# Performance work log

Measured on AMD Instinct MI355X. Metric: run time of the kernel, lower is better.

Reference implementation:

```python
import jax, jax.numpy as jnp
import numpy as np
import math

D_MODEL = 512
NUM_HEADS = 8
D_HEAD = D_MODEL // NUM_HEADS
B, S = 8, 1024


def _rel_shift(pos_score):
    # pos_score: [B, H, S, S] -> Transformer-XL relative shift
    b, h, s1, s2 = pos_score.shape
    padded = jnp.concatenate([jnp.zeros((b, h, s1, 1), pos_score.dtype), pos_score], axis=-1)
    padded = padded.reshape(b, h, s2 + 1, s1)
    return padded[:, :, 1:].reshape(b, h, s1, s2)


def setup_inputs() -> dict:
    key = jax.random.key(0)
    ks = jax.random.split(key, 16)
    scale = 1.0 / math.sqrt(D_MODEL)
    inp = {
        'query': jax.random.normal(ks[0], (B, S, D_MODEL), jnp.float32),
        'key': jax.random.normal(ks[1], (B, S, D_MODEL), jnp.float32),
        'value': jax.random.normal(ks[2], (B, S, D_MODEL), jnp.float32),
        'position_emb': jax.random.normal(ks[3], (B, S, D_MODEL), jnp.float32),
        'Wq': jax.random.normal(ks[4], (D_MODEL, D_MODEL), jnp.float32) * scale,
        'bq': jnp.zeros((D_MODEL,), jnp.float32),
        'Wk': jax.random.normal(ks[5], (D_MODEL, D_MODEL), jnp.float32) * scale,
        'bk': jnp.zeros((D_MODEL,), jnp.float32),
        'Wv': jax.random.normal(ks[6], (D_MODEL, D_MODEL), jnp.float32) * scale,
        'bv': jnp.zeros((D_MODEL,), jnp.float32),
        'Wp': jax.random.normal(ks[7], (D_MODEL, D_MODEL), jnp.float32) * scale,
        'u_bias': jax.random.normal(ks[8], (NUM_HEADS, D_HEAD), jnp.float32) * 0.1,
        'v_bias': jax.random.normal(ks[9], (NUM_HEADS, D_HEAD), jnp.float32) * 0.1,
        'Wo': jax.random.normal(ks[10], (D_MODEL, D_MODEL), jnp.float32) * scale,
        'bo': jnp.zeros((D_MODEL,), jnp.float32),
    }
    return inp


def reference(query, key, value, position_emb, Wq, bq, Wk, bk, Wv, bv, Wp, u_bias, v_bias, Wo, bo):
    b, s, _ = query.shape
    q = (query @ Wq + bq).reshape(b, s, NUM_HEADS, D_HEAD)       # [B,S,H,Dh]
    k = (key @ Wk + bk).reshape(b, s, NUM_HEADS, D_HEAD)
    v = (value @ Wv + bv).reshape(b, s, NUM_HEADS, D_HEAD)
    p = (position_emb @ Wp).reshape(b, s, NUM_HEADS, D_HEAD)
    # content score: (q + u) k^T ; pos score: (q + v) p^T with relative shift
    content_score = jnp.einsum('bqhd,bkhd->bhqk', q + u_bias, k)
    pos_score = _rel_shift(jnp.einsum('bqhd,bkhd->bhqk', q + v_bias, p))
    score = (content_score + pos_score) / math.sqrt(D_MODEL)
    atten = jax.nn.softmax(score, axis=-1)                        # dropout off (eval)
    context = jnp.einsum('bhqk,bkhd->bqhd', atten, v).reshape(b, s, D_MODEL)
    return context @ Wo + bo
```

## Files before the change

### kernel.cpp

```cpp
#include <hip/hip_runtime.h>
#include <cstdint>

typedef unsigned short ushort_t;
typedef __attribute__((ext_vector_type(8))) short bf16x8;
typedef __attribute__((ext_vector_type(4))) float f32x4;

#define S_LEN 1024
#define DHEAD 64

__device__ inline ushort_t f2bf(float f) {
    union { float f; uint32_t u; } c; c.f = f;
    uint32_t u = c.u;
    uint32_t r = u + 0x7FFFu + ((u >> 16) & 1u);
    return (ushort_t)(r >> 16);
}
__device__ inline float bf2f(ushort_t h) {
    union { uint32_t u; float f; } c; c.u = ((uint32_t)h) << 16;
    return c.f;
}
__device__ inline bf16x8 load8(const ushort_t* p) {
    union { uint4 u; bf16x8 v; } c;
    c.u = *reinterpret_cast<const uint4*>(p);
    return c.v;
}

__global__ __launch_bounds__(256) void prep_w(
    const float* __restrict__ wq, const float* __restrict__ wk,
    const float* __restrict__ wv, const float* __restrict__ wp,
    const float* __restrict__ wo, ushort_t* __restrict__ ws) {
    __shared__ float tile[64][65];
    int wi = blockIdx.z;
    const float* src = wi == 0 ? wq : wi == 1 ? wk : wi == 2 ? wv : wi == 3 ? wp : wo;
    int cx = blockIdx.x * 64, ry = blockIdx.y * 64;
    int t = threadIdx.x;
    int tr = t >> 4, tc = (t & 15) * 4;
#pragma unroll
    for (int i = 0; i < 4; i++) {
        int r = tr + i * 16;
        float4 f = *reinterpret_cast<const float4*>(src + (size_t)(ry + r) * 512 + cx + tc);
        tile[r][tc] = f.x; tile[r][tc + 1] = f.y; tile[r][tc + 2] = f.z; tile[r][tc + 3] = f.w;
    }
    __syncthreads();
    ushort_t* dst = ws + (size_t)wi * 262144;
#pragma unroll
    for (int i = 0; i < 4; i++) {
        int r = tr + i * 16;
        ushort4 o;
        o.x = f2bf(tile[tc][r]); o.y = f2bf(tile[tc + 1][r]);
        o.z = f2bf(tile[tc + 2][r]); o.w = f2bf(tile[tc + 3][r]);
        *reinterpret_cast<ushort4*>(dst + (size_t)(cx + r) * 512 + ry + tc) = o;
    }
}

__global__ __launch_bounds__(256) void prep_act(
    const float* __restrict__ q, const float* __restrict__ k,
    const float* __restrict__ v, const float* __restrict__ p,
    ushort_t* __restrict__ actb) {
    int t = blockIdx.x * 256 + threadIdx.x;
    int sec = blockIdx.y;
    const float* src = sec == 0 ? q : sec == 1 ? k : sec == 2 ? v : p;
    ushort_t* dst = actb + (size_t)sec * 4194304;
    float4 f = reinterpret_cast<const float4*>(src)[t];
    ushort4 o;
    o.x = f2bf(f.x); o.y = f2bf(f.y); o.z = f2bf(f.z); o.w = f2bf(f.w);
    *reinterpret_cast<ushort4*>(dst + (size_t)t * 4) = o;
}

template<int CVT>
__global__ __launch_bounds__(256) void proj_gemm(
    const float* __restrict__ qa, const float* __restrict__ ka,
    const float* __restrict__ va, const float* __restrict__ pa,
    const ushort_t* __restrict__ actb,
    const ushort_t* __restrict__ wT,
    const float* __restrict__ bq, const float* __restrict__ bk,
    const float* __restrict__ bv,
    const float* __restrict__ ub, const float* __restrict__ vb,
    ushort_t* __restrict__ Qu, ushort_t* __restrict__ Qv,
    ushort_t* __restrict__ Kp, ushort_t* __restrict__ Pp,
    ushort_t* __restrict__ Vt) {
    __shared__ ushort_t smem[2][128][72];
    int z = blockIdx.z;
    const float* Af = z == 0 ? qa : z == 1 ? ka : z == 2 ? pa : va;
    const ushort_t* Ab = actb + (size_t)(z == 0 ? 0 : z == 1 ? 1 : z == 2 ? 3 : 2) * 4194304;
    const ushort_t* Bt = wT + (z == 0 ? 0 : z == 1 ? 262144 : z == 2 ? 786432 : 524288);
    const float* bias = z == 0 ? bq : z == 1 ? bk : z == 3 ? bv : nullptr;

    int tid = threadIdx.x;
    int wid = tid >> 6, lane = tid & 63, quad = lane >> 4, l16 = lane & 15;
    int wr = wid >> 1, wc = wid & 1;
    int row0 = blockIdx.y * 128, col0 = blockIdx.x * 128;

    f32x4 acc[4][4];
#pragma unroll
    for (int i = 0; i < 4; i++)
#pragma unroll
        for (int j = 0; j < 4; j++) acc[i][j] = (f32x4){0.f, 0.f, 0.f, 0.f};

    for (int k0 = 0; k0 < 512; k0 += 64) {
#pragma unroll
        for (int i = 0; i < 4; i++) {
            int cid = tid + i * 256;
            int r = cid >> 3, c8 = cid & 7;
            if (CVT) {
                const float* ap = Af + (size_t)(row0 + r) * 512 + k0 + c8 * 8;
                float4 f0 = *reinterpret_cast<const float4*>(ap);
                float4 f1 = *reinterpret_cast<const float4*>(ap + 4);
                union { ushort_t s[8]; uint4 u; } pk;
                pk.s[0] = f2bf(f0.x); pk.s[1] = f2bf(f0.y); pk.s[2] = f2bf(f0.z); pk.s[3] = f2bf(f0.w);
                pk.s[4] = f2bf(f1.x); pk.s[5] = f2bf(f1.y); pk.s[6] = f2bf(f1.z); pk.s[7] = f2bf(f1.w);
                *reinterpret_cast<uint4*>(&smem[0][r][c8 * 8]) = pk.u;
            } else {
                *reinterpret_cast<uint4*>(&smem[0][r][c8 * 8]) =
                    *reinterpret_cast<const uint4*>(Ab + (size_t)(row0 + r) * 512 + k0 + c8 * 8);
            }
            *reinterpret_cast<uint4*>(&smem[1][r][c8 * 8]) =
                *reinterpret_cast<const uint4*>(Bt + (size_t)(col0 + r) * 512 + k0 + c8 * 8);
        }
        __syncthreads();
#pragma unroll
        for (int kc = 0; kc < 2; kc++) {
            bf16x8 af[4], bg[4];
#pragma unroll
            for (int m = 0; m < 4; m++)
                af[m] = load8(&smem[0][wr * 64 + m * 16 + l16][kc * 32 + quad * 8]);
#pragma unroll
            for (int n = 0; n < 4; n++)
                bg[n] = load8(&smem[1][wc * 64 + n * 16 + l16][kc * 32 + quad * 8]);
#pragma unroll
            for (int m = 0; m < 4; m++)
#pragma unroll
                for (int n = 0; n < 4; n++)
                    acc[m][n] = __builtin_amdgcn_mfma_f32_16x16x32_bf16(af[m], bg[n], acc[m][n], 0, 0, 0);
        }
        __syncthreads();
    }

    if (z == 3) {
        ushort_t (*Ts)[130] = reinterpret_cast<ushort_t(*)[130]>(&smem[0][0][0]);
#pragma unroll
        for (int m = 0; m < 4; m++)
#pragma unroll
            for (int n = 0; n < 4; n++) {
                int dl = wc * 64 + n * 16 + l16;
                float bcol = bv[col0 + dl];
#pragma unroll
                for (int r = 0; r < 4; r++) {
                    int sl = wr * 64 + m * 16 + quad * 4 + r;
                    Ts[dl][sl] = f2bf(acc[m][n][r] + bcol);
                }
            }
        __syncthreads();
        int b_ = row0 >> 10, s0 = row0 & 1023;
#pragma unroll
        for (int p = 0; p < 8; p++) {
            int dl = p * 16 + (tid >> 4);
            int sl = (tid & 15) * 8;
            int col = col0 + dl, h_ = col >> 6, d_ = col & 63;
            ushort_t* dst = Vt + (((size_t)(b_ * 8 + h_)) * 64 + d_) * 1024 + s0 + sl;
            union { uint4 u; ushort_t s[8]; } pk;
#pragma unroll
            for (int e = 0; e < 8; e++) pk.s[e] = Ts[dl][sl + e];
            *reinterpret_cast<uint4*>(dst) = pk.u;
        }
    } else {
#pragma unroll
        for (int m = 0; m < 4; m++)
#pragma unroll
            for (int n = 0; n < 4; n++) {
                int col = col0 + wc * 64 + n * 16 + l16;
                float bcol = bias ? bias[col] : 0.f;
#pragma unroll
                for (int r = 0; r < 4; r++) {
                    int row = row0 + wr * 64 + m * 16 + quad * 4 + r;
                    float val = acc[m][n][r] + bcol;
                    int b_ = row >> 10, s_ = row & 1023, h_ = col >> 6, d_ = col & 63;
                    size_t idx = (((size_t)(b_ * 8 + h_)) * 1024 + s_) * 64 + d_;
                    if (z == 0) {
                        Qu[idx] = f2bf(val + ub[col]);
                        Qv[idx] = f2bf(val + vb[col]);
                    } else {
                        (z == 1 ? Kp : Pp)[idx] = f2bf(val);
                    }
                }
            }
    }
}

__global__ __launch_bounds__(256) void out_gemm(
    const ushort_t* __restrict__ A, const ushort_t* __restrict__ Bt,
    const float* __restrict__ bias, float* __restrict__ outf) {
    __shared__ ushort_t As[128][72];
    __shared__ ushort_t Bs[64][72];
    int tid = threadIdx.x;
    int wid = tid >> 6, lane = tid & 63, quad = lane >> 4, l16 = lane & 15;
    int row0 = blockIdx.y * 128, col0 = blockIdx.x * 64;

    f32x4 acc[2][4];
#pragma unroll
    for (int i = 0; i < 2; i++)
#pragma unroll
        for (int j = 0; j < 4; j++) acc[i][j] = (f32x4){0.f, 0.f, 0.f, 0.f};

    for (int k0 = 0; k0 < 512; k0 += 64) {
#pragma unroll
        for (int i = 0; i < 4; i++) {
            int cid = tid + i * 256;
            int r = cid >> 3, c8 = cid & 7;
            *reinterpret_cast<uint4*>(&As[r][c8 * 8]) =
                *reinterpret_cast<const uint4*>(A + (size_t)(row0 + r) * 512 + k0 + c8 * 8);
        }
#pragma unroll
        for (int i = 0; i < 2; i++) {
            int cid = tid + i * 256;
            int r = cid >> 3, c8 = cid & 7;
            *reinterpret_cast<uint4*>(&Bs[r][c8 * 8]) =
                *reinterpret_cast<const uint4*>(Bt + (size_t)(col0 + r) * 512 + k0 + c8 * 8);
        }
        __syncthreads();
#pragma unroll
        for (int kc = 0; kc < 2; kc++) {
            bf16x8 af[2], bg[4];
#pragma unroll
            for (int m = 0; m < 2; m++)
                af[m] = load8(&As[wid * 32 + m * 16 + l16][kc * 32 + quad * 8]);
#pragma unroll
            for (int n = 0; n < 4; n++)
                bg[n] = load8(&Bs[n * 16 + l16][kc * 32 + quad * 8]);
#pragma unroll
            for (int m = 0; m < 2; m++)
#pragma unroll
                for (int n = 0; n < 4; n++)
                    acc[m][n] = __builtin_amdgcn_mfma_f32_16x16x32_bf16(af[m], bg[n], acc[m][n], 0, 0, 0);
        }
        __syncthreads();
    }
#pragma unroll
    for (int m = 0; m < 2; m++)
#pragma unroll
        for (int n = 0; n < 4; n++) {
            int col = col0 + n * 16 + l16;
#pragma unroll
            for (int r = 0; r < 4; r++) {
                int row = row0 + wid * 32 + m * 16 + quad * 4 + r;
                outf[(size_t)row * 512 + col] = acc[m][n][r] + bias[col];
            }
        }
}

#define POS_EMIT(B0_, B1_, WT_) do {                                          \
    f32x4 acc_ = (f32x4){0.f, 0.f, 0.f, 0.f};                                 \
    acc_ = __builtin_amdgcn_mfma_f32_16x16x32_bf16(av[0], (B0_), acc_, 0, 0, 0); \
    acc_ = __builtin_amdgcn_mfma_f32_16x16x32_bf16(av[1], (B1_), acc_, 0, 0, 0); \
    int kb_ = (WT_) + kbb;                                                    \
    if (kb_ >= kw0 && kb_ + 30 < kw1 && (WT_) + 15 <= collim) {               \
        _Pragma("unroll") for (int r_ = 0; r_ < 4; r_++) {                    \
            int m_ = quad * 4 + r_;                                           \
            sc[mtrow + m_][kb_ + m_ + l16] = f2bf(acc_[r_]);                  \
        }                                                                     \
    } else {                                                                  \
        _Pragma("unroll") for (int r_ = 0; r_ < 4; r_++) {                    \
            int m_ = quad * 4 + r_;                                           \
            int k_ = kb_ + m_ + l16;                                          \
            if (k_ >= kw0 && k_ < kw1 && ((WT_) + l16) <= collim)             \
                sc[mtrow + m_][k_] = f2bf(acc_[r_]);                          \
        }                                                                     \
    }                                                                         \
} while (0)

__device__ __forceinline__ void pos_pass(
    const ushort_t* __restrict__ P_b, ushort_t (*sc)[1032],
    const bf16x8* av, int wlo, int whi, int kbb, int collim, int mtrow,
    int kw0, int kw1, int quad, int l16) {
    if (whi < wlo) return;
    int nw = (whi - wlo) / 16 + 1;
    bf16x8 A0, A1, B0, B1;
    {
        int pr = wlo + l16; if (pr > S_LEN - 1) pr = S_LEN - 1;
        A0 = load8(P_b + (size_t)pr * 64 + quad * 8);
        A1 = load8(P_b + (size_t)pr * 64 + 32 + quad * 8);
    }
    if (nw > 1) {
        int pr = wlo + 16 + l16; if (pr > S_LEN - 1) pr = S_LEN - 1;
        B0 = load8(P_b + (size_t)pr * 64 + quad * 8);
        B1 = load8(P_b + (size_t)pr * 64 + 32 + quad * 8);
    }
    int w = 0;
    for (; w + 1 < nw; w += 2) {
        int wtA = wlo + w * 16;
        POS_EMIT(A0, A1, wtA);
        if (w + 2 < nw) {
            int pr = wtA + 32 + l16; if (pr > S_LEN - 1) pr = S_LEN - 1;
            A0 = load8(P_b + (size_t)pr * 64 + quad * 8);
            A1 = load8(P_b + (size_t)pr * 64 + 32 + quad * 8);
        }
        int wtB = wtA + 16;
        POS_EMIT(B0, B1, wtB);
        if (w + 3 < nw) {
            int pr = wtB + 32 + l16; if (pr > S_LEN - 1) pr = S_LEN - 1;
            B0 = load8(P_b + (size_t)pr * 64 + quad * 8);
            B1 = load8(P_b + (size_t)pr * 64 + 32 + quad * 8);
        }
    }
    if (w < nw) {
        int wt = wlo + w * 16;
        POS_EMIT(A0, A1, wt);
    }
}

__global__ __launch_bounds__(256, 2) void attn_kernel(
    const ushort_t* __restrict__ Qu, const ushort_t* __restrict__ Qv,
    const ushort_t* __restrict__ Kp, const ushort_t* __restrict__ Pp,
    const ushort_t* __restrict__ Vt, ushort_t* __restrict__ ctxb) {
    __shared__ ushort_t sc[32][1032];
    __shared__ float red1[4][32];
    __shared__ float red2[32][8];
    __shared__ float rowinv[32];

    constexpr float SCL = (float)(1.4426950408889634 / 22.627416997969522);

    int i = blockIdx.x;
    int bh = (i & 7) * 8 + (i >> 8);
    int q0 = ((i >> 3) & 31) << 5;

    int tid = threadIdx.x, wid = tid >> 6, lane = tid & 63;
    int quad = lane >> 4, l16 = lane & 15;

    const ushort_t* Qu_b = Qu + (size_t)bh * S_LEN * DHEAD;
    const ushort_t* Qv_b = Qv + (size_t)bh * S_LEN * DHEAD;
    const ushort_t* K_b  = Kp + (size_t)bh * S_LEN * DHEAD;
    const ushort_t* P_b  = Pp + (size_t)bh * S_LEN * DHEAD;
    const ushort_t* V_b  = Vt + (size_t)bh * DHEAD * S_LEN;

    int kw0 = wid << 8, kw1 = kw0 + 256;
    int d0 = wid << 4;

    bf16x8 au0[2], au1[2];
#pragma unroll
    for (int kc = 0; kc < 2; kc++) {
        au0[kc] = load8(Qu_b + (size_t)(q0 + l16) * 64 + kc * 32 + quad * 8);
        au1[kc] = load8(Qu_b + (size_t)(q0 + 16 + l16) * 64 + kc * 32 + quad * 8);
    }

    if (lane < 32) {
        int kz = q0 + lane + 1;
        if (kz >= kw0 && kz < kw1) sc[lane][kz] = 0;
    }

#pragma unroll
    for (int mt = 0; mt < 2; mt++) {
        int q0m = q0 + mt * 16;
        bf16x8 av1[2], av2[2];
#pragma unroll
        for (int kc = 0; kc < 2; kc++) {
            av1[kc] = load8(Qv_b + (size_t)(q0m + l16) * 64 + kc * 32 + quad * 8);
            int r2 = q0m + 1 + l16; if (r2 > S_LEN - 1) r2 = S_LEN - 1;
            av2[kc] = load8(Qv_b + (size_t)r2 * 64 + kc * 32 + quad * 8);
        }
        int wlo = (S_LEN - 16) - q0m + kw0;
        int d1 = kw1 - 1 - q0m; if (d1 > 0) d1 = 0;
        int whi = (S_LEN - 1) + d1;
        pos_pass(P_b, sc, av1, wlo, whi, q0m - (S_LEN - 1), S_LEN - 1,
                 mt * 16, kw0, kw1, quad, l16);
        int wlo2 = kw0 - q0m - 17; if (wlo2 < 0) wlo2 = 0;
        int whi2 = kw1 - 3 - q0m;
        pos_pass(P_b, sc, av2, wlo2, whi2, q0m + 2, 1 << 30,
                 mt * 16, kw0, kw1, quad, l16);
    }

    float pm0[4] = {-1e30f, -1e30f, -1e30f, -1e30f};
    float pm1[4] = {-1e30f, -1e30f, -1e30f, -1e30f};
    const ushort_t* Kw = K_b + (size_t)kw0 * 64;
#pragma unroll
    for (int nt = 0; nt < 16; ++nt) {
        const ushort_t* kp = Kw + (size_t)(nt * 16 + l16) * 64;
        bf16x8 b0 = load8(kp + quad * 8);
        bf16x8 b1 = load8(kp + 32 + quad * 8);
        int kt = kw0 + nt * 16;
        f32x4 a0, a1;
#pragma unroll
        for (int r = 0; r < 4; r++) {
            a0[r] = bf2f(sc[quad * 4 + r][kt + l16]);
            a1[r] = bf2f(sc[16 + quad * 4 + r][kt + l16]);
        }
        a0 = __builtin_amdgcn_mfma_f32_16x16x32_bf16(au0[0], b0, a0, 0, 0, 0);
        a0 = __builtin_amdgcn_mfma_f32_16x16x32_bf16(au0[1], b1, a0, 0, 0, 0);
        a1 = __builtin_amdgcn_mfma_f32_16x16x32_bf16(au1[0], b0, a1, 0, 0, 0);
        a1 = __builtin_amdgcn_mfma_f32_16x16x32_bf16(au1[1], b1, a1, 0, 0, 0);
#pragma unroll
        for (int r = 0; r < 4; r++) {
            sc[quad * 4 + r][kt + l16] = f2bf(a0[r]);
            sc[16 + quad * 4 + r][kt + l16] = f2bf(a1[r]);
            pm0[r] = fmaxf(pm0[r], a0[r]);
            pm1[r] = fmaxf(pm1[r], a1[r]);
        }
    }
#pragma unroll
    for (int off = 1; off < 16; off <<= 1)
#pragma unroll
        for (int r = 0; r < 4; r++) {
            pm0[r] = fmaxf(pm0[r], __shfl_xor(pm0[r], off));
            pm1[r] = fmaxf(pm1[r], __shfl_xor(pm1[r], off));
        }
    if (l16 == 0) {
#pragma unroll
        for (int r = 0; r < 4; r++) {
            red1[wid][quad * 4 + r] = pm0[r];
            red1[wid][16 + quad * 4 + r] = pm1[r];
        }
    }
    __syncthreads();

    int row = tid & 31, cb = tid >> 5;
    float rm = fmaxf(fmaxf(red1[0][row], red1[1][row]), fmaxf(red1[2][row], red1[3][row]));
    float ssum = 0.f;
    ushort_t* sp = &sc[row][cb * 128];
#pragma unroll
    for (int j = 0; j < 16; j++) {
        union { uint4 u; ushort_t s[8]; } in, out;
        in.u = *reinterpret_cast<uint4*>(sp + j * 8);
#pragma unroll
        for (int e = 0; e < 8; e++) {
            float ev = exp2f((bf2f(in.s[e]) - rm) * SCL);
            out.s[e] = f2bf(ev);
            ssum += ev;
        }
        *reinterpret_cast<uint4*>(sp + j * 8) = out.u;
    }
    red2[row][cb] = ssum;
    __syncthreads();
    if (tid < 32) {
        float s = 0.f;
#pragma unroll
        for (int c = 0; c < 8; c++) s += red2[tid][c];
        rowinv[tid] = 1.0f / s;
    }

    const ushort_t* Vw = V_b + (size_t)(d0 + l16) * 1024;
    f32x4 ac0 = (f32x4){0.f, 0.f, 0.f, 0.f};
    f32x4 ac1 = (f32x4){0.f, 0.f, 0.f, 0.f};
#pragma unroll
    for (int kc = 0; kc < 32; ++kc) {
        bf16x8 b = load8(Vw + kc * 32 + quad * 8);
        bf16x8 a0 = load8(&sc[l16][kc * 32 + quad * 8]);
        bf16x8 a1 = load8(&sc[16 + l16][kc * 32 + quad * 8]);
        ac0 = __builtin_amdgcn_mfma_f32_16x16x32_bf16(a0, b, ac0, 0, 0, 0);
        ac1 = __builtin_amdgcn_mfma_f32_16x16x32_bf16(a1, b, ac1, 0, 0, 0);
    }
    __syncthreads();
    int b_ = bh >> 3, h_ = bh & 7;
#pragma unroll
    for (int r = 0; r < 4; r++) {
        int m = quad * 4 + r;
        ctxb[((size_t)b_ * 1024 + (q0 + m)) * 512 + h_ * 64 + d0 + l16] =
            f2bf(ac0[r] * rowinv[m]);
        ctxb[((size_t)b_ * 1024 + (q0 + 16 + m)) * 512 + h_ * 64 + d0 + l16] =
            f2bf(ac1[r] * rowinv[16 + m]);
    }
}

extern "C" void kernel_launch(void* const* d_in, const int* in_sizes, int n_in,
                              void* d_out, int out_size, void* d_ws, size_t ws_size,
                              hipStream_t stream) {
    const float* q  = (const float*)d_in[0];
    const float* k  = (const float*)d_in[1];
    const float* v  = (const float*)d_in[2];
    const float* pe = (const float*)d_in[3];
    const float* Wq = (const float*)d_in[4];
    const float* bq = (const float*)d_in[5];
    const float* Wk = (const float*)d_in[6];
    const float* bk = (const float*)d_in[7];
    const float* Wv = (const float*)d_in[8];
    const float* bv = (const float*)d_in[9];
    const float* Wp = (const float*)d_in[10];
    const float* ub = (const float*)d_in[11];
    const float* vbias = (const float*)d_in[12];
    const float* Wo = (const float*)d_in[13];
    const float* bo = (const float*)d_in[14];
    float* out = (float*)d_out;
    ushort_t* ws = (ushort_t*)d_ws;

    ushort_t* wT  = ws;
    ushort_t* Qu  = ws + 1310720;
    ushort_t* Qv  = Qu + 4194304;
    ushort_t* Kp  = Qv + 4194304;
    ushort_t* Pp  = Kp + 4194304;
    ushort_t* Vt  = Pp + 4194304;
    ushort_t* actb = Vt + 4194304;
    ushort_t* ctx_big = actb;

    const size_t need_big = (size_t)(1310720 + 9 * 4194304) * 2;
    bool big = ws_size >= need_big;

    prep_w<<<dim3(8, 8, 5), 256, 0, stream>>>(Wq, Wk, Wv, Wp, Wo, wT);
    if (big) {
        prep_act<<<dim3(4096, 4), 256, 0, stream>>>(q, k, v, pe, actb);
        proj_gemm<0><<<dim3(4, 64, 4), 256, 0, stream>>>(q, k, v, pe, actb, wT,
            bq, bk, bv, ub, vbias, Qu, Qv, Kp, Pp, Vt);
        attn_kernel<<<2048, 256, 0, stream>>>(Qu, Qv, Kp, Pp, Vt, ctx_big);
        out_gemm<<<dim3(8, 64), 256, 0, stream>>>(ctx_big, wT + 4 * 262144, bo, out);
    } else {
        ushort_t* ctx = actb;
        proj_gemm<1><<<dim3(4, 64, 4), 256, 0, stream>>>(q, k, v, pe, nullptr, wT,
            bq, bk, bv, ub, vbias, Qu, Qv, Kp, Pp, Vt);
        attn_kernel<<<2048, 256, 0, stream>>>(Qu, Qv, Kp, Pp, Vt, ctx);
        out_gemm<<<dim3(8, 64), 256, 0, stream>>>(ctx, wT + 4 * 262144, bo, out);
    }
}
```

Baseline: 328.1 us.

## Halve attention query tile to 16 rows for higher occupancy

Measured after the change: 368.9 us. 1.12x slower.

```diff
diff --git a/kernel.cpp b/kernel.cpp
--- a/kernel.cpp
+++ b/kernel.cpp
@@ -255,21 +255,21 @@
     if (kb_ >= kw0 && kb_ + 30 < kw1 && (WT_) + 15 <= collim) {               \
         _Pragma("unroll") for (int r_ = 0; r_ < 4; r_++) {                    \
             int m_ = quad * 4 + r_;                                           \
-            sc[mtrow + m_][kb_ + m_ + l16] = f2bf(acc_[r_]);                  \
+            sc[m_][kb_ + m_ + l16] = f2bf(acc_[r_]);                          \
         }                                                                     \
     } else {                                                                  \
         _Pragma("unroll") for (int r_ = 0; r_ < 4; r_++) {                    \
             int m_ = quad * 4 + r_;                                           \
             int k_ = kb_ + m_ + l16;                                          \
             if (k_ >= kw0 && k_ < kw1 && ((WT_) + l16) <= collim)             \
-                sc[mtrow + m_][k_] = f2bf(acc_[r_]);                          \
+                sc[m_][k_] = f2bf(acc_[r_]);                                  \
         }                                                                     \
     }                                                                         \
 } while (0)
 
 __device__ __forceinline__ void pos_pass(
     const ushort_t* __restrict__ P_b, ushort_t (*sc)[1032],
-    const bf16x8* av, int wlo, int whi, int kbb, int collim, int mtrow,
+    const bf16x8* av, int wlo, int whi, int kbb, int collim,
     int kw0, int kw1, int quad, int l16) {
     if (whi < wlo) return;
     int nw = (whi - wlo) / 16 + 1;
@@ -307,20 +307,20 @@
     }
 }
 
-__global__ __launch_bounds__(256, 2) void attn_kernel(
+__global__ __launch_bounds__(256, 4) void attn_kernel(
     const ushort_t* __restrict__ Qu, const ushort_t* __restrict__ Qv,
     const ushort_t* __restrict__ Kp, const ushort_t* __restrict__ Pp,
     const ushort_t* __restrict__ Vt, ushort_t* __restrict__ ctxb) {
-    __shared__ ushort_t sc[32][1032];
-    __shared__ float red1[4][32];
-    __shared__ float red2[32][8];
-    __shared__ float rowinv[32];
+    __shared__ ushort_t sc[16][1032];
+    __shared__ float red1[4][16];
+    __shared__ float red2[16][16];
+    __shared__ float rowinv[16];
 
     constexpr float SCL = (float)(1.4426950408889634 / 22.627416997969522);
 
     int i = blockIdx.x;
-    int bh = (i & 7) * 8 + (i >> 8);
-    int q0 = ((i >> 3) & 31) << 5;
+    int bh = (i & 7) * 8 + (i >> 9);
+    int q0 = ((i >> 3) & 63) << 4;
 
     int tid = threadIdx.x, wid = tid >> 6, lane = tid & 63;
     int quad = lane >> 4, l16 = lane & 15;
@@ -334,41 +334,42 @@
     int kw0 = wid << 8, kw1 = kw0 + 256;
     int d0 = wid << 4;
 
-    bf16x8 au0[2], au1[2];
-#pragma unroll
-    for (int kc = 0; kc < 2; kc++) {
-        au0[kc] = load8(Qu_b + (size_t)(q0 + l16) * 64 + kc * 32 + quad * 8);
-        au1[kc] = load8(Qu_b + (size_t)(q0 + 16 + l16) * 64 + kc * 32 + quad * 8);
-    }
-
-    if (lane < 32) {
+    bf16x8 au[2];
+#pragma unroll
+    for (int kc = 0; kc < 2; kc++)
+        au[kc] = load8(Qu_b + (size_t)(q0 + l16) * 64 + kc * 32 + quad * 8);
+
+    if (lane < 16) {
         int kz = q0 + lane + 1;
         if (kz >= kw0 && kz < kw1) sc[lane][kz] = 0;
     }
 
-#pragma unroll
-    for (int mt = 0; mt < 2; mt++) {
-        int q0m = q0 + mt * 16;
+    {
         bf16x8 av1[2], av2[2];
 #pragma unroll
         for (int kc = 0; kc < 2; kc++) {
-            av1[kc] = load8(Qv_b + (size_t)(q0m + l16) * 64 + kc * 32 + quad * 8);
-            int r2 = q0m + 1 + l16; if (r2 > S_LEN - 1) r2 = S_LEN - 1;
+            av1[kc] = load8(Qv_b + (size_t)(q0 + l16) * 64 + kc * 32 + quad * 8);
+            int r2 = q0 + 1 + l16; if (r2 > S_LEN - 1) r2 = S_LEN - 1;
             av2[kc] = load8(Qv_b + (size_t)r2 * 64 + kc * 32 + quad * 8);
         }
-        int wlo = (S_LEN - 16) - q0m + kw0;
-        int d1 = kw1 - 1 - q0m; if (d1 > 0) d1 = 0;
+        int wlo = (S_LEN - 16) - q0 + kw0;
+        int d1 = kw1 - 1 - q0; if (d1 > 0) d1 = 0;
         int whi = (S_LEN - 1) + d1;
-        pos_pass(P_b, sc, av1, wlo, whi, q0m - (S_LEN - 1), S_LEN - 1,
-                 mt * 16, kw0, kw1, quad, l16);
-        int wlo2 = kw0 - q0m - 17; if (wlo2 < 0) wlo2 = 0;
-        int whi2 = kw1 - 3 - q0m;
-        pos_pass(P_b, sc, av2, wlo2, whi2, q0m + 2, 1 << 30,
-                 mt * 16, kw0, kw1, quad, l16);
-    }
-
-    float pm0[4] = {-1e30f, -1e30f, -1e30f, -1e30f};
-    float pm1[4] = {-1e30f, -1e30f, -1e30f, -1e30f};
+        {
+            const bf16x8* av = av1;
+            pos_pass(P_b, sc, av, wlo, whi, q0 - (S_LEN - 1), S_LEN - 1,
+                     kw0, kw1, quad, l16);
+        }
+        int wlo2 = kw0 - q0 - 17; if (wlo2 < 0) wlo2 = 0;
+        int whi2 = kw1 - 3 - q0;
+        {
+            const bf16x8* av = av2;
+            pos_pass(P_b, sc, av, wlo2, whi2, q0 + 2, 1 << 30,
+                     kw0, kw1, quad, l16);
+        }
+    }
+
+    float pm[4] = {-1e30f, -1e30f, -1e30f, -1e30f};
     const ushort_t* Kw = K_b + (size_t)kw0 * 64;
 #pragma unroll
     for (int nt = 0; nt < 16; ++nt) {
@@ -376,46 +377,33 @@
         bf16x8 b0 = load8(kp + quad * 8);
         bf16x8 b1 = load8(kp + 32 + quad * 8);
         int kt = kw0 + nt * 16;
-        f32x4 a0, a1;
-#pragma unroll
-        for (int r = 0; r < 4; r++) {
-            a0[r] = bf2f(sc[quad * 4 + r][kt + l16]);
-            a1[r] = bf2f(sc[16 + quad * 4 + r][kt + l16]);
-        }
-        a0 = __builtin_amdgcn_mfma_f32_16x16x32_bf16(au0[0], b0, a0, 0, 0, 0);
-        a0 = __builtin_amdgcn_mfma_f32_16x16x32_bf16(au0[1], b1, a0, 0, 0, 0);
-        a1 = __builtin_amdgcn_mfma_f32_16x16x32_bf16(au1[0], b0, a1, 0, 0, 0);
-        a1 = __builtin_amdgcn_mfma_f32_16x16x32_bf16(au1[1], b1, a1, 0, 0, 0);
+        f32x4 a0;
+#pragma unroll
+        for (int r = 0; r < 4; r++) a0[r] = bf2f(sc[quad * 4 + r][kt + l16]);
+        a0 = __builtin_amdgcn_mfma_f32_16x16x32_bf16(au[0], b0, a0, 0, 0, 0);
+        a0 = __builtin_amdgcn_mfma_f32_16x16x32_bf16(au[1], b1, a0, 0, 0, 0);
 #pragma unroll
         for (int r = 0; r < 4; r++) {
             sc[quad * 4 + r][kt + l16] = f2bf(a0[r]);
-            sc[16 + quad * 4 + r][kt + l16] = f2bf(a1[r]);
-            pm0[r] = fmaxf(pm0[r], a0[r]);
-            pm1[r] = fmaxf(pm1[r], a1[r]);
+            pm[r] = fmaxf(pm[r], a0[r]);
         }
     }
 #pragma unroll
     for (int off = 1; off < 16; off <<= 1)
 #pragma unroll
-        for (int r = 0; r < 4; r++) {
-            pm0[r] = fmaxf(pm0[r], __shfl_xor(pm0[r], off));
-            pm1[r] = fmaxf(pm1[r], __shfl_xor(pm1[r], off));
-        }
+        for (int r = 0; r < 4; r++) pm[r] = fmaxf(pm[r], __shfl_xor(pm[r], off));
     if (l16 == 0) {
 #pragma unroll
-        for (int r = 0; r < 4; r++) {
-            red1[wid][quad * 4 + r] = pm0[r];
-            red1[wid][16 + quad * 4 + r] = pm1[r];
-        }
+        for (int r = 0; r < 4; r++) red1[wid][quad * 4 + r] = pm[r];
     }
     __syncthreads();
 
-    int row = tid & 31, cb = tid >> 5;
+    int row = tid & 15, cb = tid >> 4;
     float rm = fmaxf(fmaxf(red1[0][row], red1[1][row]), fmaxf(red1[2][row], red1[3][row]));
     float ssum = 0.f;
-    ushort_t* sp = &sc[row][cb * 128];
-#pragma unroll
-    for (int j = 0; j < 16; j++) {
+    ushort_t* sp = &sc[row][cb * 64];
+#pragma unroll
+    for (int j = 0; j < 8; j++) {
         union { uint4 u; ushort_t s[8]; } in, out;
         in.u = *reinterpret_cast<uint4*>(sp + j * 8);
 #pragma unroll
@@ -428,23 +416,20 @@
     }
     red2[row][cb] = ssum;
     __syncthreads();
-    if (tid < 32) {
+    if (tid < 16) {
         float s = 0.f;
 #pragma unroll
-        for (int c = 0; c < 8; c++) s += red2[tid][c];
+        for (int c = 0; c < 16; c++) s += red2[tid][c];
         rowinv[tid] = 1.0f / s;
     }
 
     const ushort_t* Vw = V_b + (size_t)(d0 + l16) * 1024;
     f32x4 ac0 = (f32x4){0.f, 0.f, 0.f, 0.f};
-    f32x4 ac1 = (f32x4){0.f, 0.f, 0.f, 0.f};
 #pragma unroll
     for (int kc = 0; kc < 32; ++kc) {
         bf16x8 b = load8(Vw + kc * 32 + quad * 8);
         bf16x8 a0 = load8(&sc[l16][kc * 32 + quad * 8]);
-        bf16x8 a1 = load8(&sc[16 + l16][kc * 32 + quad * 8]);
         ac0 = __builtin_amdgcn_mfma_f32_16x16x32_bf16(a0, b, ac0, 0, 0, 0);
-        ac1 = __builtin_amdgcn_mfma_f32_16x16x32_bf16(a1, b, ac1, 0, 0, 0);
     }
     __syncthreads();
     int b_ = bh >> 3, h_ = bh & 7;
@@ -453,8 +438,6 @@
         int m = quad * 4 + r;
         ctxb[((size_t)b_ * 1024 + (q0 + m)) * 512 + h_ * 64 + d0 + l16] =
             f2bf(ac0[r] * rowinv[m]);
-        ctxb[((size_t)b_ * 1024 + (q0 + 16 + m)) * 512 + h_ * 64 + d0 + l16] =
-            f2bf(ac1[r] * rowinv[16 + m]);
     }
 }
 
@@ -496,13 +479,13 @@
         prep_act<<<dim3(4096, 4), 256, 0, stream>>>(q, k, v, pe, actb);
         proj_gemm<0><<<dim3(4, 64, 4), 256, 0, stream>>>(q, k, v, pe, actb, wT,
             bq, bk, bv, ub, vbias, Qu, Qv, Kp, Pp, Vt);
-        attn_kernel<<<2048, 256, 0, stream>>>(Qu, Qv, Kp, Pp, Vt, ctx_big);
+        attn_kernel<<<4096, 256, 0, stream>>>(Qu, Qv, Kp, Pp, Vt, ctx_big);
         out_gemm<<<dim3(8, 64), 256, 0, stream>>>(ctx_big, wT + 4 * 262144, bo, out);
     } else {
         ushort_t* ctx = actb;
         proj_gemm<1><<<dim3(4, 64, 4), 256, 0, stream>>>(q, k, v, pe, nullptr, wT,
             bq, bk, bv, ub, vbias, Qu, Qv, Kp, Pp, Vt);
-        attn_kernel<<<2048, 256, 0, stream>>>(Qu, Qv, Kp, Pp, Vt, ctx);
+        attn_kernel<<<4096, 256, 0, stream>>>(Qu, Qv, Kp, Pp, Vt, ctx);
         out_gemm<<<dim3(8, 64), 256, 0, stream>>>(ctx, wT + 4 * 262144, bo, out);
     }
 }
```
